# Performance work log

Measured on AMD Instinct MI355X. Metric: run time of the kernel, lower is better.

The kernel has to match this reference:

```python
import jax, jax.numpy as jnp
import numpy as np

DIM = 768
NUM_HEADS = 12
SMALLEST_RATIO = 0.25
LARGEST_RATIO = 1.0


def setup_inputs() -> dict:
    key = jax.random.key(0)
    k0, k1, k2 = jax.random.split(key, 3)
    B, N = 4, 2048
    x = jax.random.normal(k0, (B, N, DIM), dtype=jnp.float32)
    Wqkv = jax.random.normal(k1, (3 * DIM, DIM), dtype=jnp.float32) * 0.02
    bqkv = jnp.zeros((3 * DIM,), dtype=jnp.float32)
    Wproj = jax.random.normal(k2, (DIM, DIM), dtype=jnp.float32) * 0.02
    bproj = jnp.zeros((DIM,), dtype=jnp.float32)
    return {"x": x, "Wqkv": Wqkv, "bqkv": bqkv, "Wproj": Wproj, "bproj": bproj, "ratio": 1}


def reference(x, Wqkv, bqkv, Wproj, bproj, ratio):
    dc = int(ratio * DIM)
    # dynamic slimmable-width slicing: smallest/largest ratio take leading block,
    # intermediate ratios take trailing block
    if ratio == SMALLEST_RATIO or ratio == LARGEST_RATIO:
        wq, bq = Wqkv[: dc * 3, :dc], bqkv[: dc * 3]
        wp, bp = Wproj[:dc, :dc], bproj[:dc]
    else:
        wq, bq = Wqkv[-dc * 3 :, -dc:], bqkv[-dc * 3 :]
        wp, bp = Wproj[-dc:, -dc:], bproj[-dc:]
    B, N, C = x.shape
    hd = C // NUM_HEADS
    scale = (DIM // NUM_HEADS) ** -0.5  # set at init from full dim, not sliced C
    qkv = x @ wq.T + bq                               # [B, N, 3C]
    qkv = qkv.reshape(B, N, 3, NUM_HEADS, hd).transpose(2, 0, 3, 1, 4)  # [3,B,H,N,hd]
    q, k, v = qkv[0], qkv[1], qkv[2]
    attn = jax.nn.softmax(jnp.einsum("bhqd,bhkd->bhqk", q, k) * scale, axis=-1)
    out = jnp.einsum("bhqk,bhkd->bhqd", attn, v)      # [B,H,N,hd]
    out = out.transpose(0, 2, 1, 3).reshape(B, N, C)
    return out @ wp.T + bp
```

## Files before the change

### kernel.cpp

```cpp
#include <hip/hip_runtime.h>

typedef __bf16 bf16x8 __attribute__((ext_vector_type(8)));
typedef __bf16 bf16x2 __attribute__((ext_vector_type(2)));
typedef float  f32x4  __attribute__((ext_vector_type(4)));
typedef float  f32x16 __attribute__((ext_vector_type(16)));
typedef unsigned short u16;
typedef unsigned u32x2 __attribute__((ext_vector_type(2)));
typedef unsigned u32x4 __attribute__((ext_vector_type(4)));

__device__ __forceinline__ u16 f2bf(float f) {
  return __builtin_bit_cast(u16, (__bf16)f);
}
__device__ __forceinline__ unsigned pack2(float lo, float hi) {
  bf16x2 t;
  t[0] = (__bf16)lo; t[1] = (__bf16)hi;
  return __builtin_bit_cast(unsigned, t);
}

#define GLOAD16(g, l) __builtin_amdgcn_global_load_lds( \
    (__attribute__((address_space(1))) void*)(void*)(g), \
    (__attribute__((address_space(3))) void*)(l), 16, 0, 0)

#define QSCALE 0.18033688011112042f

__global__ __launch_bounds__(256) void cvt_bf16(const float* __restrict__ src,
                                                unsigned* __restrict__ dst, int n8) {
  int i = blockIdx.x * 256 + threadIdx.x;
  if (i >= n8) return;
  const float4* s = (const float4*)src + 2 * (size_t)i;
  float4 a = s[0], b = s[1];
  u32x4 o = {pack2(a.x, a.y), pack2(a.z, a.w), pack2(b.x, b.y), pack2(b.z, b.w)};
  *((u32x4*)dst + i) = o;
}

template<int EPI>
__global__ __launch_bounds__(256) void gemm_tn(
    const u16* __restrict__ A, const u16* __restrict__ B,
    const float* __restrict__ bias, float* __restrict__ outF,
    u16* __restrict__ qws, u16* __restrict__ kws, u16* __restrict__ vtws,
    int M, int N, int K) {
  __shared__ __align__(16) u16 As[8192];
  __shared__ __align__(16) u16 Bs[8192];
  const int tid = threadIdx.x;
  const int ln = tid & 63, wv = tid >> 6;
  const int wr = wv >> 1, wc = wv & 1;
  const int m0 = blockIdx.x * 128, n0 = blockIdx.y * 128;

  f32x4 acc[4][4] = {};

  const int c0 = tid, c1 = tid + 256;
  const int r0 = c0 >> 2, kc0 = ((c0 & 3) ^ ((r0 >> 1) & 3)) * 8;
  const int r1 = c1 >> 2, kc1 = ((c1 & 3) ^ ((r1 >> 1) & 3)) * 8;
  const u16* ag0 = A + (size_t)(m0 + r0) * K + kc0;
  const u16* ag1 = A + (size_t)(m0 + r1) * K + kc1;
  const u16* bg0 = B + (size_t)(n0 + r0) * K + kc0;
  const u16* bg1 = B + (size_t)(n0 + r1) * K + kc1;

  GLOAD16(ag0, As + wv * 512);
  GLOAD16(ag1, As + 2048 + wv * 512);
  GLOAD16(bg0, Bs + wv * 512);
  GLOAD16(bg1, Bs + 2048 + wv * 512);
  __syncthreads();

  int cur = 0;
  for (int k0 = 0; k0 < K; k0 += 32) {
    const int nxt = cur ^ 1;
    if (k0 + 32 < K) {
      GLOAD16(ag0 + k0 + 32, As + nxt * 4096 + wv * 512);
      GLOAD16(ag1 + k0 + 32, As + nxt * 4096 + 2048 + wv * 512);
      GLOAD16(bg0 + k0 + 32, Bs + nxt * 4096 + wv * 512);
      GLOAD16(bg1 + k0 + 32, Bs + nxt * 4096 + 2048 + wv * 512);
    }
    const u16* ab = As + cur * 4096;
    const u16* bb = Bs + cur * 4096;
    bf16x8 af[4], bfr[4];
#pragma unroll
    for (int i = 0; i < 4; ++i) {
      int ra = wr * 64 + i * 16 + (ln & 15);
      af[i] = *(const bf16x8*)(ab + ra * 32 + (((ln >> 4) ^ ((ra >> 1) & 3)) * 8));
      int rb = wc * 64 + i * 16 + (ln & 15);
      bfr[i] = *(const bf16x8*)(bb + rb * 32 + (((ln >> 4) ^ ((rb >> 1) & 3)) * 8));
    }
#pragma unroll
    for (int i = 0; i < 4; ++i)
#pragma unroll
      for (int j = 0; j < 4; ++j)
        acc[i][j] = __builtin_amdgcn_mfma_f32_16x16x32_bf16(af[i], bfr[j], acc[i][j], 0, 0, 0);
    __syncthreads();
    cur = nxt;
  }

  if (EPI == 1) {
#pragma unroll
    for (int j = 0; j < 4; ++j) {
      int col = n0 + wc * 64 + j * 16 + (ln & 15);
      float bj = bias[col];
#pragma unroll
      for (int i = 0; i < 4; ++i) {
        int mr = m0 + wr * 64 + i * 16 + ((ln >> 4) << 2);
#pragma unroll
        for (int r = 0; r < 4; ++r)
          outF[(size_t)(mr + r) * N + col] = acc[i][j][r] + bj;
      }
    }
  } else {
    const int s = n0 / 768;
#pragma unroll
    for (int j = 0; j < 4; ++j) {
      int col = n0 + wc * 64 + j * 16 + (ln & 15);
      float bj = bias[col];
      int ns = col - s * 768;
      int h = ns >> 6, d = ns & 63;
#pragma unroll
      for (int i = 0; i < 4; ++i) {
        int m = m0 + wr * 64 + i * 16 + ((ln >> 4) << 2);
        int b = m >> 11, iseq = m & 2047;
        size_t bh = (size_t)(b * 12 + h);
        if (s == 0) {
#pragma unroll
          for (int r = 0; r < 4; ++r)
            qws[(bh * 2048 + iseq + r) * 64 + d] = f2bf((acc[i][j][r] + bj) * QSCALE);
        } else if (s == 1) {
#pragma unroll
          for (int r = 0; r < 4; ++r)
            kws[(bh * 2048 + iseq + r) * 64 + d] = f2bf(acc[i][j][r] + bj);
        } else {
          u32x2 pk = {pack2(acc[i][j][0] + bj, acc[i][j][1] + bj),
                      pack2(acc[i][j][2] + bj, acc[i][j][3] + bj)};
          *(u32x2*)(vtws + (bh * 64 + d) * 2048 + iseq) = pk;
        }
      }
    }
  }
}

__global__ __launch_bounds__(256, 3) void attn_fa(
    const u16* __restrict__ qws, const u16* __restrict__ kws,
    const u16* __restrict__ vtws, u16* __restrict__ aows) {
  __shared__ __align__(16) u16 Ks[8192];
  __shared__ __align__(16) u16 Vs[8192];
  const int tid = threadIdx.x, ln = tid & 63, wv = tid >> 6;
  const int lq = ln & 31, hi = ln >> 5;
  const int bh = blockIdx.y;
  const int q0 = blockIdx.x * 128 + wv * 32;
  const size_t kbase = (size_t)bh * 2048 * 64;
  const size_t vbase = (size_t)bh * 64 * 2048;

  bf16x8 qf[4];
  {
    const u16* qp = qws + kbase + (size_t)(q0 + lq) * 64 + hi * 8;
#pragma unroll
    for (int dc = 0; dc < 4; ++dc) qf[dc] = *(const bf16x8*)(qp + dc * 16);
  }

  const u32x4 onesw = {0x3F803F80u, 0x3F803F80u, 0x3F803F80u, 0x3F803F80u};
  const bf16x8 ones = __builtin_bit_cast(bf16x8, onesw);
  const f32x16 zc = {};

  f32x16 o0 = {}, o1 = {};
  f32x16 lacc = {};

  int offL[4], offH[4];
#pragma unroll
  for (int dc = 0; dc < 4; ++dc) {
    const int ch = dc * 2 + hi;
    offL[dc] = lq * 64 + ((ch ^ (lq & 7)) * 8);
    offH[dc] = (32 + lq) * 64 + ((ch ^ (lq & 7)) * 8);
  }

  const int c0 = tid, c1 = tid + 256;
  const int r0 = c0 >> 3, kc0 = ((c0 & 7) ^ (r0 & 7)) * 8;
  const int r1 = c1 >> 3, kc1 = ((c1 & 7) ^ (r1 & 7)) * 8;
  const int pr0 = (r0 & ~12) | ((r0 & 4) << 1) | ((r0 & 8) >> 1);
  const int pr1 = (r1 & ~12) | ((r1 & 4) << 1) | ((r1 & 8) >> 1);
  const u16* kg0 = kws + kbase + (size_t)pr0 * 64 + kc0;
  const u16* kg1 = kws + kbase + (size_t)pr1 * 64 + kc1;
  const u16* vg0 = vtws + vbase + (size_t)r0 * 2048 + kc0;
  const u16* vg1 = vtws + vbase + (size_t)r1 * 2048 + kc1;

  GLOAD16(kg0, Ks + wv * 512);
  GLOAD16(kg1, Ks + 2048 + wv * 512);
  GLOAD16(vg0, Vs + wv * 512);
  GLOAD16(vg1, Vs + 2048 + wv * 512);
  __syncthreads();

  int cur = 0;
  for (int kb = 0; kb < 2048; kb += 64) {
    const int nxt = cur ^ 1;
    if (kb + 64 < 2048) {
      GLOAD16(kg0 + (size_t)(kb + 64) * 64, Ks + nxt * 4096 + wv * 512);
      GLOAD16(kg1 + (size_t)(kb + 64) * 64, Ks + nxt * 4096 + 2048 + wv * 512);
      GLOAD16(vg0 + kb + 64, Vs + nxt * 4096 + wv * 512);
      GLOAD16(vg1 + kb + 64, Vs + nxt * 4096 + 2048 + wv * 512);
    }
    const u16* kbuf = Ks + cur * 4096;
    const u16* vbuf = Vs + cur * 4096;

    f32x16 s0, s1;
    {
      bf16x8 ka = *(const bf16x8*)(kbuf + offL[0]);
      s0 = __builtin_amdgcn_mfma_f32_32x32x16_bf16(ka, qf[0], zc, 0, 0, 0);
      bf16x8 kb2 = *(const bf16x8*)(kbuf + offH[0]);
      s1 = __builtin_amdgcn_mfma_f32_32x32x16_bf16(kb2, qf[0], zc, 0, 0, 0);
    }
#pragma unroll
    for (int dc = 1; dc < 4; ++dc) {
      bf16x8 ka = *(const bf16x8*)(kbuf + offL[dc]);
      s0 = __builtin_amdgcn_mfma_f32_32x32x16_bf16(ka, qf[dc], s0, 0, 0, 0);
      bf16x8 kb2 = *(const bf16x8*)(kbuf + offH[dc]);
      s1 = __builtin_amdgcn_mfma_f32_32x32x16_bf16(kb2, qf[dc], s1, 0, 0, 0);
    }

#pragma unroll
    for (int r = 0; r < 16; ++r) s0[r] = __builtin_amdgcn_exp2f(s0[r]);
#pragma unroll
    for (int r = 0; r < 16; ++r) s1[r] = __builtin_amdgcn_exp2f(s1[r]);

#pragma unroll
    for (int c = 0; c < 4; ++c) {
      const f32x16& src = (c < 2) ? s0 : s1;
      const int base = (c & 1) * 8;
      u32x4 pw = {pack2(src[base + 0], src[base + 1]),
                  pack2(src[base + 2], src[base + 3]),
                  pack2(src[base + 4], src[base + 5]),
                  pack2(src[base + 6], src[base + 7])};
      bf16x8 pfrag = __builtin_bit_cast(bf16x8, pw);
      bf16x8 va = *(const bf16x8*)(vbuf + offL[c]);
      o0 = __builtin_amdgcn_mfma_f32_32x32x16_bf16(va, pfrag, o0, 0, 0, 0);
      bf16x8 vb = *(const bf16x8*)(vbuf + offH[c]);
      o1 = __builtin_amdgcn_mfma_f32_32x32x16_bf16(vb, pfrag, o1, 0, 0, 0);
      lacc = __builtin_amdgcn_mfma_f32_32x32x16_bf16(ones, pfrag, lacc, 0, 0, 0);
    }
    __syncthreads();
    cur = nxt;
  }

  const float rl = 1.0f / lacc[0];
  const int b = bh / 12, h = bh % 12;
  u16* orow = aows + (size_t)(b * 2048 + q0 + lq) * 768 + h * 64;
#pragma unroll
  for (int g = 0; g < 4; ++g) {
    u32x2 pk0 = {pack2(o0[4 * g + 0] * rl, o0[4 * g + 1] * rl),
                 pack2(o0[4 * g + 2] * rl, o0[4 * g + 3] * rl)};
    u32x2 pk1 = {pack2(o1[4 * g + 0] * rl, o1[4 * g + 1] * rl),
                 pack2(o1[4 * g + 2] * rl, o1[4 * g + 3] * rl)};
    *(u32x2*)(orow + g * 8 + 4 * hi)      = pk0;
    *(u32x2*)(orow + 32 + g * 8 + 4 * hi) = pk1;
  }
}

extern "C" void kernel_launch(void* const* d_in, const int* in_sizes, int n_in,
                              void* d_out, int out_size, void* d_ws, size_t ws_size,
                              hipStream_t stream) {
  const float* x     = (const float*)d_in[0];
  const float* Wqkv  = (const float*)d_in[1];
  const float* bqkv  = (const float*)d_in[2];
  const float* Wproj = (const float*)d_in[3];
  const float* bproj = (const float*)d_in[4];
  float* out = (float*)d_out;

  u16* xb   = (u16*)d_ws;
  u16* wqb  = xb  + 6291456;
  u16* wpb  = wqb + 1769472;
  u16* qws  = wpb + 589824;
  u16* kws  = qws + 6291456;
  u16* vtws = kws + 6291456;
  u16* aows = vtws + 6291456;

  cvt_bf16<<<6291456 / 8 / 256, 256, 0, stream>>>(x, (unsigned*)xb, 6291456 / 8);
  cvt_bf16<<<1769472 / 8 / 256, 256, 0, stream>>>(Wqkv, (unsigned*)wqb, 1769472 / 8);
  cvt_bf16<<<589824 / 8 / 256, 256, 0, stream>>>(Wproj, (unsigned*)wpb, 589824 / 8);

  gemm_tn<0><<<dim3(64, 18), 256, 0, stream>>>(xb, wqb, bqkv, nullptr,
                                               qws, kws, vtws, 8192, 2304, 768);
  attn_fa<<<dim3(16, 48), 256, 0, stream>>>(qws, kws, vtws, aows);
  gemm_tn<1><<<dim3(64, 6), 256, 0, stream>>>(aows, wpb, bproj, out,
                                              nullptr, nullptr, nullptr,
                                              8192, 768, 768);
}
```

Baseline: 148.0 us.

## Split KV range across wave pairs with 64-row Q tiles per wave

Each wave now handles 64 query rows, reusing every K/V LDS fragment for two Q groups, and the 2048-key range is split between two wave pairs that each stream half the keys into separate LDS buffers. The partial outputs and row sums are combined through LDS at the end. The ones-matrix MFMA used for row sums is replaced with scalar adds of the exponentials. The aim is fewer LDS reads per MFMA and removal of the extra row-sum MFMA. In exchange LDS use doubles, register pressure rises, occupancy drops from 3 to 2 blocks, and a cross-wave reduction step is added.

```diff
diff --git a/kernel.cpp b/kernel.cpp
--- a/kernel.cpp
+++ b/kernel.cpp
@@ -134,31 +134,32 @@
   }
 }
 
-__global__ __launch_bounds__(256, 3) void attn_fa(
+__global__ __launch_bounds__(256, 2) void attn_fa(
     const u16* __restrict__ qws, const u16* __restrict__ kws,
     const u16* __restrict__ vtws, u16* __restrict__ aows) {
-  __shared__ __align__(16) u16 Ks[8192];
-  __shared__ __align__(16) u16 Vs[8192];
+  __shared__ __align__(16) u16 Ks[16384];
+  __shared__ __align__(16) u16 Vs[16384];
   const int tid = threadIdx.x, ln = tid & 63, wv = tid >> 6;
   const int lq = ln & 31, hi = ln >> 5;
+  const int qw = wv & 1;
+  const int p  = wv >> 1;
   const int bh = blockIdx.y;
-  const int q0 = blockIdx.x * 128 + wv * 32;
+  const int q0 = blockIdx.x * 128 + qw * 64;
+  const int kv0 = p * 1024;
   const size_t kbase = (size_t)bh * 2048 * 64;
   const size_t vbase = (size_t)bh * 64 * 2048;
 
-  bf16x8 qf[4];
-  {
-    const u16* qp = qws + kbase + (size_t)(q0 + lq) * 64 + hi * 8;
-#pragma unroll
-    for (int dc = 0; dc < 4; ++dc) qf[dc] = *(const bf16x8*)(qp + dc * 16);
-  }
-
-  const u32x4 onesw = {0x3F803F80u, 0x3F803F80u, 0x3F803F80u, 0x3F803F80u};
-  const bf16x8 ones = __builtin_bit_cast(bf16x8, onesw);
+  bf16x8 qf[2][4];
+#pragma unroll
+  for (int g = 0; g < 2; ++g) {
+    const u16* qp = qws + kbase + (size_t)(q0 + g * 32 + lq) * 64 + hi * 8;
+#pragma unroll
+    for (int dc = 0; dc < 4; ++dc) qf[g][dc] = *(const bf16x8*)(qp + dc * 16);
+  }
+
   const f32x16 zc = {};
-
-  f32x16 o0 = {}, o1 = {};
-  f32x16 lacc = {};
+  f32x16 o0[2] = {}, o1[2] = {};
+  float ls0[2] = {0.f, 0.f}, ls1[2] = {0.f, 0.f};
 
   int offL[4], offH[4];
 #pragma unroll
@@ -168,84 +169,136 @@
     offH[dc] = (32 + lq) * 64 + ((ch ^ (lq & 7)) * 8);
   }
 
-  const int c0 = tid, c1 = tid + 256;
-  const int r0 = c0 >> 3, kc0 = ((c0 & 7) ^ (r0 & 7)) * 8;
-  const int r1 = c1 >> 3, kc1 = ((c1 & 7) ^ (r1 & 7)) * 8;
+  const int lt = tid & 127;
+  const int r0 = lt >> 3;
   const int pr0 = (r0 & ~12) | ((r0 & 4) << 1) | ((r0 & 8) >> 1);
-  const int pr1 = (r1 & ~12) | ((r1 & 4) << 1) | ((r1 & 8) >> 1);
-  const u16* kg0 = kws + kbase + (size_t)pr0 * 64 + kc0;
-  const u16* kg1 = kws + kbase + (size_t)pr1 * 64 + kc1;
-  const u16* vg0 = vtws + vbase + (size_t)r0 * 2048 + kc0;
-  const u16* vg1 = vtws + vbase + (size_t)r1 * 2048 + kc1;
-
-  GLOAD16(kg0, Ks + wv * 512);
-  GLOAD16(kg1, Ks + 2048 + wv * 512);
-  GLOAD16(vg0, Vs + wv * 512);
-  GLOAD16(vg1, Vs + 2048 + wv * 512);
+  const int sc = ((lt & 7) ^ (r0 & 7)) * 8;
+  const u16* kg = kws + kbase + (size_t)(kv0 + pr0) * 64 + sc;
+  const u16* vg = vtws + vbase + (size_t)r0 * 2048 + kv0 + sc;
+  u16* ksb = Ks + p * 8192;
+  u16* vsb = Vs + p * 8192;
+  const int sd = qw * 512;
+
+#pragma unroll
+  for (int j = 0; j < 4; ++j) {
+    GLOAD16(kg + j * 1024, ksb + sd + j * 1024);
+    GLOAD16(vg + (size_t)j * 32768, vsb + sd + j * 1024);
+  }
   __syncthreads();
 
   int cur = 0;
-  for (int kb = 0; kb < 2048; kb += 64) {
+  for (int kb = 0; kb < 1024; kb += 64) {
     const int nxt = cur ^ 1;
-    if (kb + 64 < 2048) {
-      GLOAD16(kg0 + (size_t)(kb + 64) * 64, Ks + nxt * 4096 + wv * 512);
-      GLOAD16(kg1 + (size_t)(kb + 64) * 64, Ks + nxt * 4096 + 2048 + wv * 512);
-      GLOAD16(vg0 + kb + 64, Vs + nxt * 4096 + wv * 512);
-      GLOAD16(vg1 + kb + 64, Vs + nxt * 4096 + 2048 + wv * 512);
-    }
-    const u16* kbuf = Ks + cur * 4096;
-    const u16* vbuf = Vs + cur * 4096;
-
-    f32x16 s0, s1;
+    if (kb + 64 < 1024) {
+#pragma unroll
+      for (int j = 0; j < 4; ++j) {
+        GLOAD16(kg + (size_t)(kb + 64) * 64 + j * 1024, ksb + nxt * 4096 + sd + j * 1024);
+        GLOAD16(vg + (kb + 64) + (size_t)j * 32768,     vsb + nxt * 4096 + sd + j * 1024);
+      }
+    }
+    const u16* kbuf = ksb + cur * 4096;
+    const u16* vbuf = vsb + cur * 4096;
+
+    f32x16 s0[2], s1[2];
     {
       bf16x8 ka = *(const bf16x8*)(kbuf + offL[0]);
-      s0 = __builtin_amdgcn_mfma_f32_32x32x16_bf16(ka, qf[0], zc, 0, 0, 0);
-      bf16x8 kb2 = *(const bf16x8*)(kbuf + offH[0]);
-      s1 = __builtin_amdgcn_mfma_f32_32x32x16_bf16(kb2, qf[0], zc, 0, 0, 0);
+      bf16x8 kh = *(const bf16x8*)(kbuf + offH[0]);
+      s0[0] = __builtin_amdgcn_mfma_f32_32x32x16_bf16(ka, qf[0][0], zc, 0, 0, 0);
+      s0[1] = __builtin_amdgcn_mfma_f32_32x32x16_bf16(ka, qf[1][0], zc, 0, 0, 0);
+      s1[0] = __builtin_amdgcn_mfma_f32_32x32x16_bf16(kh, qf[0][0], zc, 0, 0, 0);
+      s1[1] = __builtin_amdgcn_mfma_f32_32x32x16_bf16(kh, qf[1][0], zc, 0, 0, 0);
     }
 #pragma unroll
     for (int dc = 1; dc < 4; ++dc) {
       bf16x8 ka = *(const bf16x8*)(kbuf + offL[dc]);
-      s0 = __builtin_amdgcn_mfma_f32_32x32x16_bf16(ka, qf[dc], s0, 0, 0, 0);
-      bf16x8 kb2 = *(const bf16x8*)(kbuf + offH[dc]);
-      s1 = __builtin_amdgcn_mfma_f32_32x32x16_bf16(kb2, qf[dc], s1, 0, 0, 0);
-    }
-
-#pragma unroll
-    for (int r = 0; r < 16; ++r) s0[r] = __builtin_amdgcn_exp2f(s0[r]);
-#pragma unroll
-    for (int r = 0; r < 16; ++r) s1[r] = __builtin_amdgcn_exp2f(s1[r]);
+      bf16x8 kh = *(const bf16x8*)(kbuf + offH[dc]);
+      s0[0] = __builtin_amdgcn_mfma_f32_32x32x16_bf16(ka, qf[0][dc], s0[0], 0, 0, 0);
+      s0[1] = __builtin_amdgcn_mfma_f32_32x32x16_bf16(ka, qf[1][dc], s0[1], 0, 0, 0);
+      s1[0] = __builtin_amdgcn_mfma_f32_32x32x16_bf16(kh, qf[0][dc], s1[0], 0, 0, 0);
+      s1[1] = __builtin_amdgcn_mfma_f32_32x32x16_bf16(kh, qf[1][dc], s1[1], 0, 0, 0);
+    }
+
+#pragma unroll
+    for (int g = 0; g < 2; ++g) {
+      float a0 = 0.f, a1 = 0.f;
+#pragma unroll
+      for (int r = 0; r < 16; ++r) {
+        float e = __builtin_amdgcn_exp2f(s0[g][r]); s0[g][r] = e; a0 += e;
+      }
+#pragma unroll
+      for (int r = 0; r < 16; ++r) {
+        float e = __builtin_amdgcn_exp2f(s1[g][r]); s1[g][r] = e; a1 += e;
+      }
+      ls0[g] += a0; ls1[g] += a1;
+    }
 
 #pragma unroll
     for (int c = 0; c < 4; ++c) {
-      const f32x16& src = (c < 2) ? s0 : s1;
-      const int base = (c & 1) * 8;
-      u32x4 pw = {pack2(src[base + 0], src[base + 1]),
-                  pack2(src[base + 2], src[base + 3]),
-                  pack2(src[base + 4], src[base + 5]),
-                  pack2(src[base + 6], src[base + 7])};
-      bf16x8 pfrag = __builtin_bit_cast(bf16x8, pw);
       bf16x8 va = *(const bf16x8*)(vbuf + offL[c]);
-      o0 = __builtin_amdgcn_mfma_f32_32x32x16_bf16(va, pfrag, o0, 0, 0, 0);
       bf16x8 vb = *(const bf16x8*)(vbuf + offH[c]);
-      o1 = __builtin_amdgcn_mfma_f32_32x32x16_bf16(vb, pfrag, o1, 0, 0, 0);
-      lacc = __builtin_amdgcn_mfma_f32_32x32x16_bf16(ones, pfrag, lacc, 0, 0, 0);
+#pragma unroll
+      for (int g = 0; g < 2; ++g) {
+        const f32x16& src = (c < 2) ? s0[g] : s1[g];
+        const int base = (c & 1) * 8;
+        u32x4 pw = {pack2(src[base + 0], src[base + 1]),
+                    pack2(src[base + 2], src[base + 3]),
+                    pack2(src[base + 4], src[base + 5]),
+                    pack2(src[base + 6], src[base + 7])};
+        bf16x8 pfrag = __builtin_bit_cast(bf16x8, pw);
+        o0[g] = __builtin_amdgcn_mfma_f32_32x32x16_bf16(va, pfrag, o0[g], 0, 0, 0);
+        o1[g] = __builtin_amdgcn_mfma_f32_32x32x16_bf16(vb, pfrag, o1[g], 0, 0, 0);
+      }
     }
     __syncthreads();
     cur = nxt;
   }
 
-  const float rl = 1.0f / lacc[0];
-  const int b = bh / 12, h = bh % 12;
-  u16* orow = aows + (size_t)(b * 2048 + q0 + lq) * 768 + h * 64;
-#pragma unroll
-  for (int g = 0; g < 4; ++g) {
-    u32x2 pk0 = {pack2(o0[4 * g + 0] * rl, o0[4 * g + 1] * rl),
-                 pack2(o0[4 * g + 2] * rl, o0[4 * g + 3] * rl)};
-    u32x2 pk1 = {pack2(o1[4 * g + 0] * rl, o1[4 * g + 1] * rl),
-                 pack2(o1[4 * g + 2] * rl, o1[4 * g + 3] * rl)};
-    *(u32x2*)(orow + g * 8 + 4 * hi)      = pk0;
-    *(u32x2*)(orow + 32 + g * 8 + 4 * hi) = pk1;
+  float lg[2];
+#pragma unroll
+  for (int g = 0; g < 2; ++g) {
+    lg[g] = ls0[g] + ls1[g];
+    lg[g] += __shfl_xor(lg[g], 32);
+  }
+
+  float* ex = (float*)(qw ? Vs : Ks);
+  if (wv >= 2) {
+    float* w = ex + ln * 66;
+#pragma unroll
+    for (int r = 0; r < 16; ++r) {
+      w[r]      = o0[0][r];
+      w[16 + r] = o1[0][r];
+      w[32 + r] = o0[1][r];
+      w[48 + r] = o1[1][r];
+    }
+    w[64] = lg[0]; w[65] = lg[1];
+  }
+  __syncthreads();
+  if (wv < 2) {
+    const float* w = ex + ln * 66;
+#pragma unroll
+    for (int r = 0; r < 16; ++r) {
+      o0[0][r] += w[r];
+      o1[0][r] += w[16 + r];
+      o0[1][r] += w[32 + r];
+      o1[1][r] += w[48 + r];
+    }
+    lg[0] += w[64]; lg[1] += w[65];
+
+    const int b = bh / 12, h = bh % 12;
+#pragma unroll
+    for (int g = 0; g < 2; ++g) {
+      const float rl = 1.0f / lg[g];
+      u16* orow = aows + (size_t)(b * 2048 + q0 + g * 32 + lq) * 768 + h * 64;
+#pragma unroll
+      for (int t = 0; t < 4; ++t) {
+        u32x2 pk0 = {pack2(o0[g][4 * t + 0] * rl, o0[g][4 * t + 1] * rl),
+                     pack2(o0[g][4 * t + 2] * rl, o0[g][4 * t + 3] * rl)};
+        u32x2 pk1 = {pack2(o1[g][4 * t + 0] * rl, o1[g][4 * t + 1] * rl),
+                     pack2(o1[g][4 * t + 2] * rl, o1[g][4 * t + 3] * rl)};
+        *(u32x2*)(orow + t * 8 + 4 * hi)      = pk0;
+        *(u32x2*)(orow + 32 + t * 8 + 4 * hi) = pk1;
+      }
+    }
   }
 }
 
```

New measurement: 147.7 us. Within noise of the previous version (-0.2%).

## Split attention KV range across waves with per-wave pipelined loads and XCD mapping

Applied to the files above, without the earlier changes.

Restructures the attention kernel so each block handles 32 queries, with each of its four waves covering a quarter of the KV sequence using private LDS buffers, a 3-stage software pipeline and no per-iteration block barriers. Partial outputs and row sums are reduced through LDS at the end. It also replaces the ones-MFMA row sum with scalar adds, retiles V^T storage to suit the new loads, remaps blocks so each XCD handles a fixed set of heads, and fuses the three conversion kernels into one. The aim is to remove __syncthreads stalls and improve L2 locality, at the cost of a final cross-wave reduction, more LDS per block and lower occupancy.

```diff
diff --git a/kernel.cpp b/kernel.cpp
--- a/kernel.cpp
+++ b/kernel.cpp
@@ -23,10 +23,20 @@
 
 #define QSCALE 0.18033688011112042f
 
-__global__ __launch_bounds__(256) void cvt_bf16(const float* __restrict__ src,
-                                                unsigned* __restrict__ dst, int n8) {
+__global__ __launch_bounds__(256) void cvt_all(
+    const float* __restrict__ x, const float* __restrict__ wq,
+    const float* __restrict__ wp, unsigned* __restrict__ xb,
+    unsigned* __restrict__ wqb, unsigned* __restrict__ wpb) {
   int i = blockIdx.x * 256 + threadIdx.x;
-  if (i >= n8) return;
+  const float* src;
+  unsigned* dst;
+  if (i < 786432) {
+    src = x; dst = xb;
+  } else if (i < 786432 + 221184) {
+    src = wq; dst = wqb; i -= 786432;
+  } else {
+    src = wp; dst = wpb; i -= 786432 + 221184;
+  }
   const float4* s = (const float4*)src + 2 * (size_t)i;
   float4 a = s[0], b = s[1];
   u32x4 o = {pack2(a.x, a.y), pack2(a.z, a.w), pack2(b.x, b.y), pack2(b.z, b.w)};
@@ -127,24 +137,28 @@
         } else {
           u32x2 pk = {pack2(acc[i][j][0] + bj, acc[i][j][1] + bj),
                       pack2(acc[i][j][2] + bj, acc[i][j][3] + bj)};
-          *(u32x2*)(vtws + (bh * 64 + d) * 2048 + iseq) = pk;
+          *(u32x2*)(vtws + ((size_t)bh * 64 + (iseq >> 5)) * 2048 +
+                    ((iseq >> 3) & 3) * 512 + (size_t)d * 8 + (iseq & 7)) = pk;
         }
       }
     }
   }
 }
 
-__global__ __launch_bounds__(256, 3) void attn_fa(
+__global__ __launch_bounds__(256, 2) void attn_fa(
     const u16* __restrict__ qws, const u16* __restrict__ kws,
     const u16* __restrict__ vtws, u16* __restrict__ aows) {
-  __shared__ __align__(16) u16 Ks[8192];
-  __shared__ __align__(16) u16 Vs[8192];
+  __shared__ __align__(16) u16 SM[40960];
   const int tid = threadIdx.x, ln = tid & 63, wv = tid >> 6;
   const int lq = ln & 31, hi = ln >> 5;
-  const int bh = blockIdx.y;
-  const int q0 = blockIdx.x * 128 + wv * 32;
+
+  const int flat = blockIdx.y * 64 + blockIdx.x;
+  const int xcd = flat & 7, jj = flat >> 3;
+  const int bh = xcd * 6 + (jj % 6);
+  const int q0 = (jj / 6) * 32;
+
+  const int kv0 = wv * 512;
   const size_t kbase = (size_t)bh * 2048 * 64;
-  const size_t vbase = (size_t)bh * 64 * 2048;
 
   bf16x8 qf[4];
   {
@@ -153,99 +167,145 @@
     for (int dc = 0; dc < 4; ++dc) qf[dc] = *(const bf16x8*)(qp + dc * 16);
   }
 
-  const u32x4 onesw = {0x3F803F80u, 0x3F803F80u, 0x3F803F80u, 0x3F803F80u};
-  const bf16x8 ones = __builtin_bit_cast(bf16x8, onesw);
   const f32x16 zc = {};
-
   f32x16 o0 = {}, o1 = {};
-  f32x16 lacc = {};
-
-  int offL[4], offH[4];
-#pragma unroll
-  for (int dc = 0; dc < 4; ++dc) {
-    const int ch = dc * 2 + hi;
-    offL[dc] = lq * 64 + ((ch ^ (lq & 7)) * 8);
-    offH[dc] = (32 + lq) * 64 + ((ch ^ (lq & 7)) * 8);
-  }
-
-  const int c0 = tid, c1 = tid + 256;
-  const int r0 = c0 >> 3, kc0 = ((c0 & 7) ^ (r0 & 7)) * 8;
-  const int r1 = c1 >> 3, kc1 = ((c1 & 7) ^ (r1 & 7)) * 8;
-  const int pr0 = (r0 & ~12) | ((r0 & 4) << 1) | ((r0 & 8) >> 1);
-  const int pr1 = (r1 & ~12) | ((r1 & 4) << 1) | ((r1 & 8) >> 1);
-  const u16* kg0 = kws + kbase + (size_t)pr0 * 64 + kc0;
-  const u16* kg1 = kws + kbase + (size_t)pr1 * 64 + kc1;
-  const u16* vg0 = vtws + vbase + (size_t)r0 * 2048 + kc0;
-  const u16* vg1 = vtws + vbase + (size_t)r1 * 2048 + kc1;
-
-  GLOAD16(kg0, Ks + wv * 512);
-  GLOAD16(kg1, Ks + 2048 + wv * 512);
-  GLOAD16(vg0, Vs + wv * 512);
-  GLOAD16(vg1, Vs + 2048 + wv * 512);
+  float lsum = 0.f;
+
+  int koff[4], voff[2];
+#pragma unroll
+  for (int dc = 0; dc < 4; ++dc)
+    koff[dc] = lq * 64 + (((dc * 2 + hi) ^ (lq & 7)) * 8);
+#pragma unroll
+  for (int c = 0; c < 2; ++c)
+    voff[c] = (c * 2 + hi) * 512 + lq * 8;
+
+  const int r0 = ln >> 3;
+  const int chs = ((ln & 7) ^ r0) * 8;
+  const int pib = (r0 & 3) | ((r0 & 4) << 1);
+  const u16* kgb = kws + kbase + (size_t)(kv0 + pib) * 64 + chs;
+  const u16* vg  = vtws + ((size_t)bh * 64 + (kv0 >> 5)) * 2048 + (size_t)ln * 8;
+  u16* Kw = SM + wv * 10240;
+  u16* Vw = Kw + 4096;
+  const int dst = ln * 8;
+
+#define STAGE_K(buf, t) do { \
+    GLOAD16(kgb + (size_t)(t) * 2048,        Kw + (buf) * 2048 + dst); \
+    GLOAD16(kgb + (size_t)(t) * 2048 + 256,  Kw + (buf) * 2048 + 512 + dst); \
+    GLOAD16(kgb + (size_t)(t) * 2048 + 1024, Kw + (buf) * 2048 + 1024 + dst); \
+    GLOAD16(kgb + (size_t)(t) * 2048 + 1280, Kw + (buf) * 2048 + 1536 + dst); \
+  } while (0)
+#define STAGE_V(buf, t) do { \
+    GLOAD16(vg + (size_t)(t) * 2048,        Vw + (buf) * 2048 + dst); \
+    GLOAD16(vg + (size_t)(t) * 2048 + 512,  Vw + (buf) * 2048 + 512 + dst); \
+    GLOAD16(vg + (size_t)(t) * 2048 + 1024, Vw + (buf) * 2048 + 1024 + dst); \
+    GLOAD16(vg + (size_t)(t) * 2048 + 1536, Vw + (buf) * 2048 + 1536 + dst); \
+  } while (0)
+
+#define QKEXP(PW0, PW1) do { \
+    const u16* kb_ = Kw + kq * 2048; \
+    bf16x8 kf0 = *(const bf16x8*)(kb_ + koff[0]); \
+    f32x16 s_ = __builtin_amdgcn_mfma_f32_32x32x16_bf16(kf0, qf[0], zc, 0, 0, 0); \
+    bf16x8 kf1 = *(const bf16x8*)(kb_ + koff[1]); \
+    s_ = __builtin_amdgcn_mfma_f32_32x32x16_bf16(kf1, qf[1], s_, 0, 0, 0); \
+    bf16x8 kf2 = *(const bf16x8*)(kb_ + koff[2]); \
+    s_ = __builtin_amdgcn_mfma_f32_32x32x16_bf16(kf2, qf[2], s_, 0, 0, 0); \
+    bf16x8 kf3 = *(const bf16x8*)(kb_ + koff[3]); \
+    s_ = __builtin_amdgcn_mfma_f32_32x32x16_bf16(kf3, qf[3], s_, 0, 0, 0); \
+    float a_ = 0.f, b_ = 0.f; \
+    _Pragma("unroll") \
+    for (int r = 0; r < 16; r += 2) { \
+      float e0 = __builtin_amdgcn_exp2f(s_[r]);     s_[r] = e0;     a_ += e0; \
+      float e1 = __builtin_amdgcn_exp2f(s_[r + 1]); s_[r + 1] = e1; b_ += e1; \
+    } \
+    lsum += a_ + b_; \
+    PW0 = (u32x4){pack2(s_[0], s_[1]),   pack2(s_[2], s_[3]), \
+                  pack2(s_[4], s_[5]),   pack2(s_[6], s_[7])}; \
+    PW1 = (u32x4){pack2(s_[8], s_[9]),   pack2(s_[10], s_[11]), \
+                  pack2(s_[12], s_[13]), pack2(s_[14], s_[15])}; \
+  } while (0)
+
+#define PVSTEP(PR0, PR1) do { \
+    const u16* vb_ = Vw + vp * 2048; \
+    bf16x8 va0 = *(const bf16x8*)(vb_ + voff[0]); \
+    bf16x8 vb0 = *(const bf16x8*)(vb_ + voff[0] + 256); \
+    bf16x8 va1 = *(const bf16x8*)(vb_ + voff[1]); \
+    bf16x8 vb1 = *(const bf16x8*)(vb_ + voff[1] + 256); \
+    o0 = __builtin_amdgcn_mfma_f32_32x32x16_bf16(va0, __builtin_bit_cast(bf16x8, PR0), o0, 0, 0, 0); \
+    o1 = __builtin_amdgcn_mfma_f32_32x32x16_bf16(vb0, __builtin_bit_cast(bf16x8, PR0), o1, 0, 0, 0); \
+    o0 = __builtin_amdgcn_mfma_f32_32x32x16_bf16(va1, __builtin_bit_cast(bf16x8, PR1), o0, 0, 0, 0); \
+    o1 = __builtin_amdgcn_mfma_f32_32x32x16_bf16(vb1, __builtin_bit_cast(bf16x8, PR1), o1, 0, 0, 0); \
+  } while (0)
+
+#define BODY(PR0, PR1, PW0, PW1, DOSTAGE) do { \
+    asm volatile("s_waitcnt vmcnt(4)" ::: "memory"); \
+    if (DOSTAGE) { STAGE_K(ks, t + 2); STAGE_V(vs, t + 2); } \
+    QKEXP(PW0, PW1); \
+    PVSTEP(PR0, PR1); \
+    kq ^= 1; ks ^= 1; vp = (vp == 2) ? 0 : vp + 1; vs = (vs == 2) ? 0 : vs + 1; \
+    ++t; \
+  } while (0)
+
+  u32x4 pA0, pA1, pB0, pB1;
+
+  STAGE_K(0, 0);
+  STAGE_V(0, 0);
+  STAGE_K(1, 1);
+  STAGE_V(1, 1);
+  asm volatile("s_waitcnt vmcnt(12)" ::: "memory");
+  int t = 0, kq = 0, ks = 0, vp = 0, vs = 2;
+  QKEXP(pA0, pA1);
+  kq = 1;
+
+  for (int i = 0; i < 7; ++i) {
+    BODY(pA0, pA1, pB0, pB1, 1);
+    BODY(pB0, pB1, pA0, pA1, 1);
+  }
+  BODY(pA0, pA1, pB0, pB1, 0);
+  asm volatile("s_waitcnt vmcnt(0)" ::: "memory");
+  PVSTEP(pB0, pB1);
+#undef BODY
+#undef PVSTEP
+#undef QKEXP
+#undef STAGE_V
+#undef STAGE_K
+
+  float lg = lsum + __shfl_xor(lsum, 32);
+
   __syncthreads();
-
-  int cur = 0;
-  for (int kb = 0; kb < 2048; kb += 64) {
-    const int nxt = cur ^ 1;
-    if (kb + 64 < 2048) {
-      GLOAD16(kg0 + (size_t)(kb + 64) * 64, Ks + nxt * 4096 + wv * 512);
-      GLOAD16(kg1 + (size_t)(kb + 64) * 64, Ks + nxt * 4096 + 2048 + wv * 512);
-      GLOAD16(vg0 + kb + 64, Vs + nxt * 4096 + wv * 512);
-      GLOAD16(vg1 + kb + 64, Vs + nxt * 4096 + 2048 + wv * 512);
-    }
-    const u16* kbuf = Ks + cur * 4096;
-    const u16* vbuf = Vs + cur * 4096;
-
-    f32x16 s0, s1;
-    {
-      bf16x8 ka = *(const bf16x8*)(kbuf + offL[0]);
-      s0 = __builtin_amdgcn_mfma_f32_32x32x16_bf16(ka, qf[0], zc, 0, 0, 0);
-      bf16x8 kb2 = *(const bf16x8*)(kbuf + offH[0]);
-      s1 = __builtin_amdgcn_mfma_f32_32x32x16_bf16(kb2, qf[0], zc, 0, 0, 0);
-    }
-#pragma unroll
-    for (int dc = 1; dc < 4; ++dc) {
-      bf16x8 ka = *(const bf16x8*)(kbuf + offL[dc]);
-      s0 = __builtin_amdgcn_mfma_f32_32x32x16_bf16(ka, qf[dc], s0, 0, 0, 0);
-      bf16x8 kb2 = *(const bf16x8*)(kbuf + offH[dc]);
-      s1 = __builtin_amdgcn_mfma_f32_32x32x16_bf16(kb2, qf[dc], s1, 0, 0, 0);
-    }
-
-#pragma unroll
-    for (int r = 0; r < 16; ++r) s0[r] = __builtin_amdgcn_exp2f(s0[r]);
-#pragma unroll
-    for (int r = 0; r < 16; ++r) s1[r] = __builtin_amdgcn_exp2f(s1[r]);
-
-#pragma unroll
-    for (int c = 0; c < 4; ++c) {
-      const f32x16& src = (c < 2) ? s0 : s1;
-      const int base = (c & 1) * 8;
-      u32x4 pw = {pack2(src[base + 0], src[base + 1]),
-                  pack2(src[base + 2], src[base + 3]),
-                  pack2(src[base + 4], src[base + 5]),
-                  pack2(src[base + 6], src[base + 7])};
-      bf16x8 pfrag = __builtin_bit_cast(bf16x8, pw);
-      bf16x8 va = *(const bf16x8*)(vbuf + offL[c]);
-      o0 = __builtin_amdgcn_mfma_f32_32x32x16_bf16(va, pfrag, o0, 0, 0, 0);
-      bf16x8 vb = *(const bf16x8*)(vbuf + offH[c]);
-      o1 = __builtin_amdgcn_mfma_f32_32x32x16_bf16(vb, pfrag, o1, 0, 0, 0);
-      lacc = __builtin_amdgcn_mfma_f32_32x32x16_bf16(ones, pfrag, lacc, 0, 0, 0);
-    }
-    __syncthreads();
-    cur = nxt;
-  }
-
-  const float rl = 1.0f / lacc[0];
-  const int b = bh / 12, h = bh % 12;
-  u16* orow = aows + (size_t)(b * 2048 + q0 + lq) * 768 + h * 64;
-#pragma unroll
-  for (int g = 0; g < 4; ++g) {
-    u32x2 pk0 = {pack2(o0[4 * g + 0] * rl, o0[4 * g + 1] * rl),
-                 pack2(o0[4 * g + 2] * rl, o0[4 * g + 3] * rl)};
-    u32x2 pk1 = {pack2(o1[4 * g + 0] * rl, o1[4 * g + 1] * rl),
-                 pack2(o1[4 * g + 2] * rl, o1[4 * g + 3] * rl)};
-    *(u32x2*)(orow + g * 8 + 4 * hi)      = pk0;
-    *(u32x2*)(orow + 32 + g * 8 + 4 * hi) = pk1;
+  float* ex = (float*)SM;
+  if (wv > 0) {
+    float* w = ex + (wv - 1) * 2112 + ln;
+#pragma unroll
+    for (int r = 0; r < 16; ++r) {
+      w[r * 64]        = o0[r];
+      w[(16 + r) * 64] = o1[r];
+    }
+    ex[6336 + (wv - 1) * 64 + ln] = lg;
+  }
+  __syncthreads();
+  if (wv == 0) {
+#pragma unroll
+    for (int w2 = 0; w2 < 3; ++w2) {
+      const float* w = ex + w2 * 2112 + ln;
+#pragma unroll
+      for (int r = 0; r < 16; ++r) {
+        o0[r] += w[r * 64];
+        o1[r] += w[(16 + r) * 64];
+      }
+      lg += ex[6336 + w2 * 64 + ln];
+    }
+    const float rl = 1.0f / lg;
+    const int b = bh / 12, h = bh % 12;
+    u16* orow = aows + (size_t)(b * 2048 + q0 + lq) * 768 + h * 64;
+#pragma unroll
+    for (int t2 = 0; t2 < 4; ++t2) {
+      u32x2 pk0 = {pack2(o0[4 * t2 + 0] * rl, o0[4 * t2 + 1] * rl),
+                   pack2(o0[4 * t2 + 2] * rl, o0[4 * t2 + 3] * rl)};
+      u32x2 pk1 = {pack2(o1[4 * t2 + 0] * rl, o1[4 * t2 + 1] * rl),
+                   pack2(o1[4 * t2 + 2] * rl, o1[4 * t2 + 3] * rl)};
+      *(u32x2*)(orow + t2 * 8 + 4 * hi)      = pk0;
+      *(u32x2*)(orow + 32 + t2 * 8 + 4 * hi) = pk1;
+    }
   }
 }
 
@@ -267,13 +327,12 @@
   u16* vtws = kws + 6291456;
   u16* aows = vtws + 6291456;
 
-  cvt_bf16<<<6291456 / 8 / 256, 256, 0, stream>>>(x, (unsigned*)xb, 6291456 / 8);
-  cvt_bf16<<<1769472 / 8 / 256, 256, 0, stream>>>(Wqkv, (unsigned*)wqb, 1769472 / 8);
-  cvt_bf16<<<589824 / 8 / 256, 256, 0, stream>>>(Wproj, (unsigned*)wpb, 589824 / 8);
+  cvt_all<<<4224, 256, 0, stream>>>(x, Wqkv, Wproj,
+                                    (unsigned*)xb, (unsigned*)wqb, (unsigned*)wpb);
 
   gemm_tn<0><<<dim3(64, 18), 256, 0, stream>>>(xb, wqb, bqkv, nullptr,
                                                qws, kws, vtws, 8192, 2304, 768);
-  attn_fa<<<dim3(16, 48), 256, 0, stream>>>(qws, kws, vtws, aows);
+  attn_fa<<<dim3(64, 48), 256, 0, stream>>>(qws, kws, vtws, aows);
   gemm_tn<1><<<dim3(64, 6), 256, 0, stream>>>(aows, wpb, bproj, out,
                                               nullptr, nullptr, nullptr,
                                               8192, 768, 768);
```

New measurement: 157.5 us. +6.4%, slower.
